# Kernel tuning notes

Measured on AMD Instinct MI355X. Metric: run time of the kernel, lower is better.

Reference implementation:

```python
import jax, jax.numpy as jnp
import numpy as np

PAD_TOKEN_ID = 0
EPS = 1e-12  # torch F.normalize eps

B_Q, L_Q = 64, 32
B_D, L_D = 512, 256
HID, OUT = 768, 128
VOCAB = 30522


def setup_inputs() -> dict:
    key = jax.random.key(0)
    k1, k2, k3, k4, k5 = jax.random.split(key, 5)
    return {
        "q_hidden": jax.random.normal(k1, (B_Q, L_Q, HID), dtype=jnp.float32),
        "d_hidden": jax.random.normal(k2, (B_D, L_D, HID), dtype=jnp.float32),
        "d_input_ids": jax.random.randint(k3, (B_D, L_D), 0, VOCAB, dtype=jnp.int32),
        "skiplist": jax.random.randint(k4, (64,), 0, VOCAB, dtype=jnp.int32),
        "W": jax.random.normal(k5, (OUT, HID), dtype=jnp.float32) * (HID ** -0.5),
    }


def _l2norm(x):
    n = jnp.sqrt(jnp.sum(x * x, axis=-1, keepdims=True))
    return x / jnp.maximum(n, EPS)


def reference(q_hidden, d_hidden, d_input_ids, skiplist, W):
    # query(): linear proj + L2 normalize      (B_q, L_q, F)
    Q = _l2norm(jnp.einsum("blh,fh->blf", q_hidden, W))
    # doc(): linear proj + L2 normalize + mask (B_d, L_d, F)
    D = _l2norm(jnp.einsum("blh,fh->blf", d_hidden, W))
    is_pad = d_input_ids == PAD_TOKEN_ID
    is_punct = jnp.any(d_input_ids[..., None] == skiplist, axis=-1)
    d_mask = (~is_pad) & (~is_punct)                     # (B_d, L_d)
    D = D * d_mask[..., None].astype(D.dtype)
    # forward(): reshape to (B, N, L, F) with B = min(B_q, B_d)
    B = min(q_hidden.shape[0], d_hidden.shape[0])
    Qr = Q.reshape(B, -1, L_Q, OUT)                      # (B, 1, L_q, F)
    Dr = D.reshape(B, -1, L_D, OUT)                      # (B, N_p, L_d, F)
    Mr = d_mask.reshape(B, -1, L_D)                      # (B, N_p, L_d)
    # similarity(): cosine MaxSim, Q @ D^T with broadcast over N_p
    sim = jnp.einsum("bqf,bndf->bnqd", Qr[:, 0], Dr)     # (B, N_p, L_q, L_d)
    sim = jnp.where(Mr[:, :, None, :], sim, -jnp.inf)
    sms = jnp.max(sim, axis=-1).mean(axis=-1)            # (B, N_p)
    return sms
```

## Files before the change

### kernel.cpp

```cpp
#include <hip/hip_runtime.h>
#include <stdint.h>

typedef float  f32x4 __attribute__((ext_vector_type(4)));
typedef short  s16x8 __attribute__((ext_vector_type(8)));
typedef unsigned int u32;
typedef unsigned short u16;
typedef unsigned int u32x4 __attribute__((ext_vector_type(4)));

#define HID 768
#define OUTF 128
#define LQ 32
#define LD 256

__device__ __forceinline__ u32 pk_rna(float lo, float hi) {
    u32 a = __builtin_bit_cast(u32, lo) + 0x8000u;
    u32 b = __builtin_bit_cast(u32, hi) + 0x8000u;
    return __builtin_amdgcn_perm(b, a, 0x07060302u);
}
__device__ __forceinline__ u16 f2bf(float x) {
    return (u16)((__builtin_bit_cast(u32, x) + 0x8000u) >> 16);
}
__device__ __forceinline__ s16x8 cvt8(f32x4 lo, f32x4 hi) {
    union { u32 u[4]; s16x8 v; } ua;
    ua.u[0] = pk_rna(lo[0], lo[1]);
    ua.u[1] = pk_rna(lo[2], lo[3]);
    ua.u[2] = pk_rna(hi[0], hi[1]);
    ua.u[3] = pk_rna(hi[2], hi[3]);
    return ua.v;
}

__global__ __launch_bounds__(256) void wconv(const float* __restrict__ W,
                                             u32* __restrict__ Wb3d) {
    int t = blockIdx.x * 256 + threadIdx.x;
    int j2   = t & 3;
    int lane = (t >> 2) & 63;
    int cf   = (t >> 8) & 7;
    int kk   = t >> 11;
    int l15 = lane & 15, g4 = lane >> 4;
    int f = cf * 16 + l15;
    int k = kk * 32 + g4 * 8 + j2 * 2;
    const float* src = W + (size_t)f * HID + k;
    Wb3d[t] = pk_rna(src[0], src[1]);
}

__global__ __launch_bounds__(256) void qproj(const float* __restrict__ qh,
                                             const u16* __restrict__ Wb3,
                                             u16* __restrict__ Qb) {
    const int b = blockIdx.x;
    const int tid = threadIdx.x;
    const int w = tid >> 6, lane = tid & 63, g = lane >> 4, l15 = lane & 15;

    f32x4 acc[2][2] = {};
    const float* A0 = qh + ((size_t)b * LQ + l15) * HID + g * 8;
    const float* A1 = A0 + 16 * HID;
    const u16* Bp = Wb3 + w * 1024 + lane * 8;

    for (int kk = 0; kk < 24; ++kk) {
        f32x4 x0 = *(const f32x4*)A0;
        f32x4 x1 = *(const f32x4*)(A0 + 4);
        f32x4 y0 = *(const f32x4*)A1;
        f32x4 y1 = *(const f32x4*)(A1 + 4);
        s16x8 b0 = *(const s16x8*)(Bp);
        s16x8 b1 = *(const s16x8*)(Bp + 512);
        s16x8 a0 = cvt8(x0, x1);
        s16x8 a1 = cvt8(y0, y1);
        acc[0][0] = __builtin_amdgcn_mfma_f32_16x16x32_bf16(a0, b0, acc[0][0], 0, 0, 0);
        acc[0][1] = __builtin_amdgcn_mfma_f32_16x16x32_bf16(a0, b1, acc[0][1], 0, 0, 0);
        acc[1][0] = __builtin_amdgcn_mfma_f32_16x16x32_bf16(a1, b0, acc[1][0], 0, 0, 0);
        acc[1][1] = __builtin_amdgcn_mfma_f32_16x16x32_bf16(a1, b1, acc[1][1], 0, 0, 0);
        A0 += 32; A1 += 32; Bp += 4096;
    }

    __shared__ float part[4][32];
    __shared__ float invl[32];
#pragma unroll
    for (int rf = 0; rf < 2; ++rf)
#pragma unroll
        for (int reg = 0; reg < 4; ++reg) {
            float ss = acc[rf][0][reg] * acc[rf][0][reg] + acc[rf][1][reg] * acc[rf][1][reg];
            ss += __shfl_xor(ss, 1); ss += __shfl_xor(ss, 2);
            ss += __shfl_xor(ss, 4); ss += __shfl_xor(ss, 8);
            if (l15 == 0) part[w][rf * 16 + g * 4 + reg] = ss;
        }
    __syncthreads();
    if (tid < 32) {
        float ss = part[0][tid] + part[1][tid] + part[2][tid] + part[3][tid];
        invl[tid] = 1.f / fmaxf(sqrtf(ss), 1e-12f);
    }
    __syncthreads();
#pragma unroll
    for (int rf = 0; rf < 2; ++rf)
#pragma unroll
        for (int cf = 0; cf < 2; ++cf)
#pragma unroll
            for (int reg = 0; reg < 4; ++reg) {
                int q = rf * 16 + g * 4 + reg;
                int f = w * 32 + cf * 16 + l15;
                Qb[(size_t)b * LQ * OUTF + q * OUTF + f] = f2bf(acc[rf][cf][reg] * invl[q]);
            }
}

__global__ __launch_bounds__(512, 2) void dmax(const float* __restrict__ dh,
                                               const int* __restrict__ ids,
                                               const int* __restrict__ skiplist,
                                               const u16* __restrict__ Wb3,
                                               const u16* __restrict__ Qb,
                                               float* __restrict__ out) {
    const int bid = blockIdx.x;
    const int tid = threadIdx.x;
    const int w = tid >> 6, lane = tid & 63, g4 = lane >> 4, l15 = lane & 15;
    const int qh_ = w >> 2;

    __shared__ __align__(16) u16 stg[3][12288];
    __shared__ __align__(16) u16 outb[2][2048];
    __shared__ __align__(16) float nrm[2][16][8];
    __shared__ float red[8][16];
    __shared__ int ms[512];
    __shared__ int sk[64];

#define PADOF(v) (((v) / 192) * 1536 + (((((v) % 192)) * 8) ^ ((((v) / 192) & 7) << 4)))
    const int pad0 = PADOF(2 * tid), pad1 = PADOF(2 * tid + 1024), pad2 = PADOF(2 * tid + 2048);

    const int swz = (l15 & 7) << 4, sw45 = swz & 48, sw6 = swz & 64;
    const int aoffE = l15 * 1536 + ((g4 * 16) ^ sw45) + sw6;
    const int aoffO = l15 * 1536 + ((g4 * 16) ^ sw45) + 64 - sw6;
    const int doffE = l15 * 256 + ((g4 * 16) ^ sw45) + sw6;
    const int doffO = l15 * 256 + ((g4 * 16) ^ sw45) + 64 - sw6;

    f32x4 LA0, LA1, LA2, LA3, LA4, LA5, LB0, LB1, LB2, LB3, LB4, LB5,
          LC0, LC1, LC2, LC3, LC4, LC5;
    s16x8 Qr0, Qr1, Qr2, Qr3;
    float rmaxH[4] = {-INFINITY, -INFINITY, -INFINITY, -INFINITY};

#define SLABBASE(sab) ((const char*)dh + (size_t)(bid + (((sab) >> 4) << 8)) * 786432 \
                       + (size_t)((sab) & 15) * 49152)

#define LISSUE(sab, S) { const char* gb_ = SLABBASE(sab) + 32 * tid; \
    S##0 = *(const f32x4*)(gb_);          S##1 = *(const f32x4*)(gb_ + 16); \
    S##2 = *(const f32x4*)(gb_ + 16384);  S##3 = *(const f32x4*)(gb_ + 16400); \
    S##4 = *(const f32x4*)(gb_ + 32768);  S##5 = *(const f32x4*)(gb_ + 32784); }

#define WSTORE(P, S) { char* sb_ = (char*)&stg[P][0]; u32x4 q_; \
    q_[0] = pk_rna(S##0[0], S##0[1]); q_[1] = pk_rna(S##0[2], S##0[3]); \
    q_[2] = pk_rna(S##1[0], S##1[1]); q_[3] = pk_rna(S##1[2], S##1[3]); \
    *(u32x4*)(sb_ + pad0) = q_; \
    q_[0] = pk_rna(S##2[0], S##2[1]); q_[1] = pk_rna(S##2[2], S##2[3]); \
    q_[2] = pk_rna(S##3[0], S##3[1]); q_[3] = pk_rna(S##3[2], S##3[3]); \
    *(u32x4*)(sb_ + pad1) = q_; \
    q_[0] = pk_rna(S##4[0], S##4[1]); q_[1] = pk_rna(S##4[2], S##4[3]); \
    q_[2] = pk_rna(S##5[0], S##5[1]); q_[3] = pk_rna(S##5[2], S##5[3]); \
    *(u32x4*)(sb_ + pad2) = q_; }

#define QLOAD(doc_) { const u16* qp_ = Qb + (size_t)((bid + (doc_) * 256) >> 3) * 4096 \
                      + (qh_ * 16 + l15) * 128 + g4 * 8; \
    Qr0 = *(const s16x8*)(qp_);      Qr1 = *(const s16x8*)(qp_ + 32); \
    Qr2 = *(const s16x8*)(qp_ + 64); Qr3 = *(const s16x8*)(qp_ + 96); }

#define GEMMN(P, s_) { \
    const char* Ab_ = (const char*)&stg[P][0]; \
    u16* ob_ = &outb[(s_) & 1][0]; \
    f32x4 ac0_ = {}, ac1_ = {}; \
    _Pragma("unroll") for (int kkp = 0; kkp < 12; ++kkp) { \
        s16x8 ae_ = *(const s16x8*)(Ab_ + aoffE + kkp * 128); \
        s16x8 ao_ = *(const s16x8*)(Ab_ + aoffO + kkp * 128); \
        ac0_ = __builtin_amdgcn_mfma_f32_16x16x32_bf16(ae_, Bf[2 * kkp],     ac0_, 0, 0, 0); \
        ac1_ = __builtin_amdgcn_mfma_f32_16x16x32_bf16(ao_, Bf[2 * kkp + 1], ac1_, 0, 0, 0); \
    } \
    f32x4 aG_ = ac0_ + ac1_; \
    _Pragma("unroll") for (int rg = 0; rg < 4; ++rg) { \
        float ss_ = aG_[rg] * aG_[rg]; \
        ss_ += __shfl_xor(ss_, 1); ss_ += __shfl_xor(ss_, 2); \
        ss_ += __shfl_xor(ss_, 4); ss_ += __shfl_xor(ss_, 8); \
        if (l15 == 0) nrm[(s_) & 1][g4 * 4 + rg][w] = ss_; \
        int dr_ = g4 * 4 + rg; \
        int of_ = (dr_ * 256 + (w * 16 + l15) * 2) ^ ((dr_ & 7) << 4); \
        *(u16*)((char*)ob_ + of_) = f2bf(aG_[rg]); \
    } }

#define TAIL(sb) { \
    if ((w & 3) == ((sb) & 3)) { \
        const char* Db_ = (const char*)&outb[(sb) & 1][0]; \
        s16x8 d0_ = *(const s16x8*)(Db_ + doffE); \
        s16x8 d1_ = *(const s16x8*)(Db_ + doffO); \
        s16x8 d2_ = *(const s16x8*)(Db_ + doffE + 128); \
        s16x8 d3_ = *(const s16x8*)(Db_ + doffO + 128); \
        f32x4 s2_ = {}; \
        s2_ = __builtin_amdgcn_mfma_f32_16x16x32_bf16(Qr0, d0_, s2_, 0, 0, 0); \
        s2_ = __builtin_amdgcn_mfma_f32_16x16x32_bf16(Qr1, d1_, s2_, 0, 0, 0); \
        s2_ = __builtin_amdgcn_mfma_f32_16x16x32_bf16(Qr2, d2_, s2_, 0, 0, 0); \
        s2_ = __builtin_amdgcn_mfma_f32_16x16x32_bf16(Qr3, d3_, s2_, 0, 0, 0); \
        f32x4 n0_ = *(const f32x4*)&nrm[(sb) & 1][l15][0]; \
        f32x4 n1_ = *(const f32x4*)&nrm[(sb) & 1][l15][4]; \
        float ssv_ = (n0_[0] + n0_[1] + n0_[2] + n0_[3]) \
                   + (n1_[0] + n1_[1] + n1_[2] + n1_[3]); \
        float inv_ = 1.f / fmaxf(sqrtf(ssv_), 1e-12f); \
        int keep_ = ms[(((sb) >> 4) << 8) + (((sb) & 15) << 4) + l15]; \
        _Pragma("unroll") for (int rg = 0; rg < 4; ++rg) { \
            float v_ = keep_ ? s2_[rg] * inv_ : -INFINITY; \
            rmaxH[rg] = fmaxf(rmaxH[rg], v_); } \
    } \
    if (((sb) & 15) == 15) { \
        _Pragma("unroll") for (int rg = 0; rg < 4; ++rg) { \
            float v_ = rmaxH[rg]; \
            v_ = fmaxf(v_, __shfl_xor(v_, 1)); v_ = fmaxf(v_, __shfl_xor(v_, 2)); \
            v_ = fmaxf(v_, __shfl_xor(v_, 4)); v_ = fmaxf(v_, __shfl_xor(v_, 8)); \
            if (l15 == 0) red[w][g4 * 4 + rg] = v_; \
            rmaxH[rg] = -INFINITY; } \
        asm volatile("s_waitcnt lgkmcnt(0)" ::: "memory"); \
        __builtin_amdgcn_s_barrier(); \
        if (tid < 32) { \
            int qi_ = tid & 15; \
            int base_ = (tid < 16) ? 0 : 4; \
            float m_ = fmaxf(fmaxf(red[base_][qi_], red[base_ + 1][qi_]), \
                             fmaxf(red[base_ + 2][qi_], red[base_ + 3][qi_])); \
            m_ += __shfl_xor(m_, 1); m_ += __shfl_xor(m_, 2); \
            m_ += __shfl_xor(m_, 4); m_ += __shfl_xor(m_, 8); \
            m_ += __shfl_xor(m_, 16); \
            if (tid == 0) out[bid + (((sb) >> 4) << 8)] = m_ * (1.f / 32.f); } \
        if ((sb) == 15) { QLOAD(1); } \
    } }

#define SLABSTEP(s_, PG_, PW_, RN_, RW_, doIssue_, doWr_) { \
    if (doIssue_) LISSUE((s_) + 3, RN_); \
    GEMMN(PG_, s_); \
    if (doWr_) WSTORE(PW_, RW_); \
    asm volatile("s_waitcnt lgkmcnt(0)" ::: "memory"); \
    __builtin_amdgcn_s_barrier(); \
    TAIL(s_); }

    LISSUE(0, LA);
    LISSUE(1, LB);
    LISSUE(2, LC);

    s16x8 Bf[24];
#pragma unroll
    for (int kk = 0; kk < 24; ++kk)
        Bf[kk] = *(const s16x8*)(Wb3 + (size_t)(kk * 8 + w) * 512 + lane * 8);

    if (tid < 64) sk[tid] = skiplist[tid];
    asm volatile("s_waitcnt lgkmcnt(0)" ::: "memory");
    __builtin_amdgcn_s_barrier();
    {
        int d_ = tid >> 8, r_ = tid & 255;
        int id_ = ids[(size_t)(bid + d_ * 256) * 256 + r_];
        int keep_ = (id_ != 0);
#pragma unroll
        for (int j = 0; j < 64; ++j) keep_ &= (id_ != sk[j]);
        ms[tid] = keep_;
    }
    WSTORE(0, LA);
    QLOAD(0);
    asm volatile("s_waitcnt lgkmcnt(0)" ::: "memory");
    __builtin_amdgcn_s_barrier();

    for (int j = 0; j < 10; ++j) {
        const int s0 = 3 * j;
        SLABSTEP(s0,     0, 1, LA, LB, true,        true);
        SLABSTEP(s0 + 1, 1, 2, LB, LC, true,        true);
        SLABSTEP(s0 + 2, 2, 0, LC, LA, s0 + 5 < 32, true);
    }
    SLABSTEP(30, 0, 1, LA, LB, false, true);
    SLABSTEP(31, 1, 2, LB, LC, false, false);
}

extern "C" void kernel_launch(void* const* d_in, const int* in_sizes, int n_in,
                              void* d_out, int out_size, void* d_ws, size_t ws_size,
                              hipStream_t stream) {
    const float* q_hidden = (const float*)d_in[0];
    const float* d_hidden = (const float*)d_in[1];
    const int*   d_ids    = (const int*)d_in[2];
    const int*   skiplist = (const int*)d_in[3];
    const float* W        = (const float*)d_in[4];
    float* out = (float*)d_out;

    u16* Wb3 = (u16*)d_ws;
    u16* Qb  = (u16*)((char*)d_ws + 256 * 1024);

    wconv<<<192, 256, 0, stream>>>(W, (u32*)Wb3);
    qproj<<<64, 256, 0, stream>>>(q_hidden, Wb3, Qb);
    dmax<<<256, 512, 0, stream>>>(d_hidden, d_ids, skiplist, Wb3, Qb, out);
}
```

Measured before the change: 102.9 us.

## Process slabs in pairs with four LDS stages to halve barriers

Restructures the dmax main loop from a three-stage one-slab-per-barrier pipeline to a four-buffer scheme that stages, projects and scores two slabs per barrier interval. Global loads for the next pair are issued while the current pair is projected, and the per-document max reduction moves out into a separate FLUSH step. This aims to cut the number of workgroup barriers per slab and give more independent MFMA work between syncs. In exchange it uses more LDS (four staging buffers), which may limit occupancy at two blocks per CU, and it keeps fewer register-held prefetches in flight.

```diff
diff --git a/kernel.cpp b/kernel.cpp
--- a/kernel.cpp
+++ b/kernel.cpp
@@ -111,9 +111,9 @@
     const int w = tid >> 6, lane = tid & 63, g4 = lane >> 4, l15 = lane & 15;
     const int qh_ = w >> 2;
 
-    __shared__ __align__(16) u16 stg[3][12288];
-    __shared__ __align__(16) u16 outb[2][2048];
-    __shared__ __align__(16) float nrm[2][16][8];
+    __shared__ __align__(16) u16 stg[4][12288];
+    __shared__ __align__(16) u16 outb[4][2048];
+    __shared__ __align__(16) float nrm[4][16][8];
     __shared__ float red[8][16];
     __shared__ int ms[512];
     __shared__ int sk[64];
@@ -127,8 +127,7 @@
     const int doffE = l15 * 256 + ((g4 * 16) ^ sw45) + sw6;
     const int doffO = l15 * 256 + ((g4 * 16) ^ sw45) + 64 - sw6;
 
-    f32x4 LA0, LA1, LA2, LA3, LA4, LA5, LB0, LB1, LB2, LB3, LB4, LB5,
-          LC0, LC1, LC2, LC3, LC4, LC5;
+    f32x4 LA0, LA1, LA2, LA3, LA4, LA5, LB0, LB1, LB2, LB3, LB4, LB5;
     s16x8 Qr0, Qr1, Qr2, Qr3;
     float rmaxH[4] = {-INFINITY, -INFINITY, -INFINITY, -INFINITY};
 
@@ -156,9 +155,9 @@
     Qr0 = *(const s16x8*)(qp_);      Qr1 = *(const s16x8*)(qp_ + 32); \
     Qr2 = *(const s16x8*)(qp_ + 64); Qr3 = *(const s16x8*)(qp_ + 96); }
 
-#define GEMMN(P, s_) { \
+#define GEMMN(P, OB) { \
     const char* Ab_ = (const char*)&stg[P][0]; \
-    u16* ob_ = &outb[(s_) & 1][0]; \
+    u16* ob_ = &outb[OB][0]; \
     f32x4 ac0_ = {}, ac1_ = {}; \
     _Pragma("unroll") for (int kkp = 0; kkp < 12; ++kkp) { \
         s16x8 ae_ = *(const s16x8*)(Ab_ + aoffE + kkp * 128); \
@@ -171,15 +170,15 @@
         float ss_ = aG_[rg] * aG_[rg]; \
         ss_ += __shfl_xor(ss_, 1); ss_ += __shfl_xor(ss_, 2); \
         ss_ += __shfl_xor(ss_, 4); ss_ += __shfl_xor(ss_, 8); \
-        if (l15 == 0) nrm[(s_) & 1][g4 * 4 + rg][w] = ss_; \
+        if (l15 == 0) nrm[OB][g4 * 4 + rg][w] = ss_; \
         int dr_ = g4 * 4 + rg; \
         int of_ = (dr_ * 256 + (w * 16 + l15) * 2) ^ ((dr_ & 7) << 4); \
         *(u16*)((char*)ob_ + of_) = f2bf(aG_[rg]); \
     } }
 
-#define TAIL(sb) { \
-    if ((w & 3) == ((sb) & 3)) { \
-        const char* Db_ = (const char*)&outb[(sb) & 1][0]; \
+#define TAILP(sb, OB, PR) { \
+    if ((w & 3) == (PR)) { \
+        const char* Db_ = (const char*)&outb[OB][0]; \
         s16x8 d0_ = *(const s16x8*)(Db_ + doffE); \
         s16x8 d1_ = *(const s16x8*)(Db_ + doffO); \
         s16x8 d2_ = *(const s16x8*)(Db_ + doffE + 128); \
@@ -189,8 +188,8 @@
         s2_ = __builtin_amdgcn_mfma_f32_16x16x32_bf16(Qr1, d1_, s2_, 0, 0, 0); \
         s2_ = __builtin_amdgcn_mfma_f32_16x16x32_bf16(Qr2, d2_, s2_, 0, 0, 0); \
         s2_ = __builtin_amdgcn_mfma_f32_16x16x32_bf16(Qr3, d3_, s2_, 0, 0, 0); \
-        f32x4 n0_ = *(const f32x4*)&nrm[(sb) & 1][l15][0]; \
-        f32x4 n1_ = *(const f32x4*)&nrm[(sb) & 1][l15][4]; \
+        f32x4 n0_ = *(const f32x4*)&nrm[OB][l15][0]; \
+        f32x4 n1_ = *(const f32x4*)&nrm[OB][l15][4]; \
         float ssv_ = (n0_[0] + n0_[1] + n0_[2] + n0_[3]) \
                    + (n1_[0] + n1_[1] + n1_[2] + n1_[3]); \
         float inv_ = 1.f / fmaxf(sqrtf(ssv_), 1e-12f); \
@@ -198,39 +197,29 @@
         _Pragma("unroll") for (int rg = 0; rg < 4; ++rg) { \
             float v_ = keep_ ? s2_[rg] * inv_ : -INFINITY; \
             rmaxH[rg] = fmaxf(rmaxH[rg], v_); } \
-    } \
-    if (((sb) & 15) == 15) { \
-        _Pragma("unroll") for (int rg = 0; rg < 4; ++rg) { \
-            float v_ = rmaxH[rg]; \
-            v_ = fmaxf(v_, __shfl_xor(v_, 1)); v_ = fmaxf(v_, __shfl_xor(v_, 2)); \
-            v_ = fmaxf(v_, __shfl_xor(v_, 4)); v_ = fmaxf(v_, __shfl_xor(v_, 8)); \
-            if (l15 == 0) red[w][g4 * 4 + rg] = v_; \
-            rmaxH[rg] = -INFINITY; } \
-        asm volatile("s_waitcnt lgkmcnt(0)" ::: "memory"); \
-        __builtin_amdgcn_s_barrier(); \
-        if (tid < 32) { \
-            int qi_ = tid & 15; \
-            int base_ = (tid < 16) ? 0 : 4; \
-            float m_ = fmaxf(fmaxf(red[base_][qi_], red[base_ + 1][qi_]), \
-                             fmaxf(red[base_ + 2][qi_], red[base_ + 3][qi_])); \
-            m_ += __shfl_xor(m_, 1); m_ += __shfl_xor(m_, 2); \
-            m_ += __shfl_xor(m_, 4); m_ += __shfl_xor(m_, 8); \
-            m_ += __shfl_xor(m_, 16); \
-            if (tid == 0) out[bid + (((sb) >> 4) << 8)] = m_ * (1.f / 32.f); } \
-        if ((sb) == 15) { QLOAD(1); } \
     } }
 
-#define SLABSTEP(s_, PG_, PW_, RN_, RW_, doIssue_, doWr_) { \
-    if (doIssue_) LISSUE((s_) + 3, RN_); \
-    GEMMN(PG_, s_); \
-    if (doWr_) WSTORE(PW_, RW_); \
+#define FLUSH(doc_) { \
+    _Pragma("unroll") for (int rg = 0; rg < 4; ++rg) { \
+        float v_ = rmaxH[rg]; \
+        v_ = fmaxf(v_, __shfl_xor(v_, 1)); v_ = fmaxf(v_, __shfl_xor(v_, 2)); \
+        v_ = fmaxf(v_, __shfl_xor(v_, 4)); v_ = fmaxf(v_, __shfl_xor(v_, 8)); \
+        if (l15 == 0) red[w][g4 * 4 + rg] = v_; \
+        rmaxH[rg] = -INFINITY; } \
     asm volatile("s_waitcnt lgkmcnt(0)" ::: "memory"); \
     __builtin_amdgcn_s_barrier(); \
-    TAIL(s_); }
+    if (tid < 32) { \
+        int qi_ = tid & 15; \
+        int base_ = (tid < 16) ? 0 : 4; \
+        float m_ = fmaxf(fmaxf(red[base_][qi_], red[base_ + 1][qi_]), \
+                         fmaxf(red[base_ + 2][qi_], red[base_ + 3][qi_])); \
+        m_ += __shfl_xor(m_, 1); m_ += __shfl_xor(m_, 2); \
+        m_ += __shfl_xor(m_, 4); m_ += __shfl_xor(m_, 8); \
+        m_ += __shfl_xor(m_, 16); \
+        if (tid == 0) out[bid + (doc_) * 256] = m_ * (1.f / 32.f); } }
 
     LISSUE(0, LA);
     LISSUE(1, LB);
-    LISSUE(2, LC);
 
     s16x8 Bf[24];
 #pragma unroll
@@ -249,18 +238,44 @@
         ms[tid] = keep_;
     }
     WSTORE(0, LA);
+    WSTORE(1, LB);
+    LISSUE(2, LA);
+    LISSUE(3, LB);
     QLOAD(0);
     asm volatile("s_waitcnt lgkmcnt(0)" ::: "memory");
     __builtin_amdgcn_s_barrier();
 
-    for (int j = 0; j < 10; ++j) {
-        const int s0 = 3 * j;
-        SLABSTEP(s0,     0, 1, LA, LB, true,        true);
-        SLABSTEP(s0 + 1, 1, 2, LB, LC, true,        true);
-        SLABSTEP(s0 + 2, 2, 0, LC, LA, s0 + 5 < 32, true);
-    }
-    SLABSTEP(30, 0, 1, LA, LB, false, true);
-    SLABSTEP(31, 1, 2, LB, LC, false, false);
+    for (int j = 0; j < 8; ++j) {
+        if (j > 0) {
+            TAILP(4 * j - 2, 2, 2);
+            TAILP(4 * j - 1, 3, 3);
+        }
+        WSTORE(2, LA);
+        WSTORE(3, LB);
+        if (j < 7) { LISSUE(4 * j + 4, LA); LISSUE(4 * j + 5, LB); }
+        GEMMN(0, 0);
+        GEMMN(1, 1);
+        asm volatile("s_waitcnt lgkmcnt(0)" ::: "memory");
+        __builtin_amdgcn_s_barrier();
+
+        if (j == 4) { FLUSH(0); QLOAD(1); }
+        TAILP(4 * j, 0, 0);
+        TAILP(4 * j + 1, 1, 1);
+        if (j < 7) {
+            WSTORE(0, LA);
+            WSTORE(1, LB);
+            LISSUE(4 * j + 6, LA);
+            LISSUE(4 * j + 7, LB);
+        }
+        GEMMN(2, 2);
+        GEMMN(3, 3);
+        asm volatile("s_waitcnt lgkmcnt(0)" ::: "memory");
+        __builtin_amdgcn_s_barrier();
+    }
+
+    TAILP(30, 2, 2);
+    TAILP(31, 3, 3);
+    FLUSH(1);
 }
 
 extern "C" void kernel_launch(void* const* d_in, const int* in_sizes, int n_in,
```

After: 107.1 us. +4.1%, slower.

## Shrink doc-slab pipeline from triple to double buffering in dmax

Applied to the files above, without the earlier changes.

Replaces the three register sets and three LDS staging buffers for the d_hidden slab pipeline with one register set and two LDS buffers. Each step now runs the GEMM on the current buffer, converts and stores the next slab into the other buffer, then issues the global load for the slab two ahead, with sched_barriers fixing the order. This saves 36 VGPRs and 24 KB of LDS, which may ease register pressure or allow more residency. The cost is a shorter prefetch distance, so global load latency is less well hidden.

```diff
diff --git a/kernel.cpp b/kernel.cpp
--- a/kernel.cpp
+++ b/kernel.cpp
@@ -111,7 +111,7 @@
     const int w = tid >> 6, lane = tid & 63, g4 = lane >> 4, l15 = lane & 15;
     const int qh_ = w >> 2;
 
-    __shared__ __align__(16) u16 stg[3][12288];
+    __shared__ __align__(16) u16 stg[2][12288];
     __shared__ __align__(16) u16 outb[2][2048];
     __shared__ __align__(16) float nrm[2][16][8];
     __shared__ float red[8][16];
@@ -127,28 +127,27 @@
     const int doffE = l15 * 256 + ((g4 * 16) ^ sw45) + sw6;
     const int doffO = l15 * 256 + ((g4 * 16) ^ sw45) + 64 - sw6;
 
-    f32x4 LA0, LA1, LA2, LA3, LA4, LA5, LB0, LB1, LB2, LB3, LB4, LB5,
-          LC0, LC1, LC2, LC3, LC4, LC5;
+    f32x4 LA0, LA1, LA2, LA3, LA4, LA5;
     s16x8 Qr0, Qr1, Qr2, Qr3;
     float rmaxH[4] = {-INFINITY, -INFINITY, -INFINITY, -INFINITY};
 
 #define SLABBASE(sab) ((const char*)dh + (size_t)(bid + (((sab) >> 4) << 8)) * 786432 \
                        + (size_t)((sab) & 15) * 49152)
 
-#define LISSUE(sab, S) { const char* gb_ = SLABBASE(sab) + 32 * tid; \
-    S##0 = *(const f32x4*)(gb_);          S##1 = *(const f32x4*)(gb_ + 16); \
-    S##2 = *(const f32x4*)(gb_ + 16384);  S##3 = *(const f32x4*)(gb_ + 16400); \
-    S##4 = *(const f32x4*)(gb_ + 32768);  S##5 = *(const f32x4*)(gb_ + 32784); }
-
-#define WSTORE(P, S) { char* sb_ = (char*)&stg[P][0]; u32x4 q_; \
-    q_[0] = pk_rna(S##0[0], S##0[1]); q_[1] = pk_rna(S##0[2], S##0[3]); \
-    q_[2] = pk_rna(S##1[0], S##1[1]); q_[3] = pk_rna(S##1[2], S##1[3]); \
+#define LISSUE(sab) { const char* gb_ = SLABBASE(sab) + 32 * tid; \
+    LA0 = *(const f32x4*)(gb_);          LA1 = *(const f32x4*)(gb_ + 16); \
+    LA2 = *(const f32x4*)(gb_ + 16384);  LA3 = *(const f32x4*)(gb_ + 16400); \
+    LA4 = *(const f32x4*)(gb_ + 32768);  LA5 = *(const f32x4*)(gb_ + 32784); }
+
+#define WSTORE(P) { char* sb_ = (char*)&stg[P][0]; u32x4 q_; \
+    q_[0] = pk_rna(LA0[0], LA0[1]); q_[1] = pk_rna(LA0[2], LA0[3]); \
+    q_[2] = pk_rna(LA1[0], LA1[1]); q_[3] = pk_rna(LA1[2], LA1[3]); \
     *(u32x4*)(sb_ + pad0) = q_; \
-    q_[0] = pk_rna(S##2[0], S##2[1]); q_[1] = pk_rna(S##2[2], S##2[3]); \
-    q_[2] = pk_rna(S##3[0], S##3[1]); q_[3] = pk_rna(S##3[2], S##3[3]); \
+    q_[0] = pk_rna(LA2[0], LA2[1]); q_[1] = pk_rna(LA2[2], LA2[3]); \
+    q_[2] = pk_rna(LA3[0], LA3[1]); q_[3] = pk_rna(LA3[2], LA3[3]); \
     *(u32x4*)(sb_ + pad1) = q_; \
-    q_[0] = pk_rna(S##4[0], S##4[1]); q_[1] = pk_rna(S##4[2], S##4[3]); \
-    q_[2] = pk_rna(S##5[0], S##5[1]); q_[3] = pk_rna(S##5[2], S##5[3]); \
+    q_[0] = pk_rna(LA4[0], LA4[1]); q_[1] = pk_rna(LA4[2], LA4[3]); \
+    q_[2] = pk_rna(LA5[0], LA5[1]); q_[3] = pk_rna(LA5[2], LA5[3]); \
     *(u32x4*)(sb_ + pad2) = q_; }
 
 #define QLOAD(doc_) { const u16* qp_ = Qb + (size_t)((bid + (doc_) * 256) >> 3) * 4096 \
@@ -220,17 +219,17 @@
         if ((sb) == 15) { QLOAD(1); } \
     } }
 
-#define SLABSTEP(s_, PG_, PW_, RN_, RW_, doIssue_, doWr_) { \
-    if (doIssue_) LISSUE((s_) + 3, RN_); \
+#define SLABSTEP(s_, PG_) { \
     GEMMN(PG_, s_); \
-    if (doWr_) WSTORE(PW_, RW_); \
+    __builtin_amdgcn_sched_barrier(0); \
+    if ((s_) + 1 < 32) WSTORE(((s_) + 1) & 1); \
+    __builtin_amdgcn_sched_barrier(0); \
+    if ((s_) + 2 < 32) LISSUE((s_) + 2); \
     asm volatile("s_waitcnt lgkmcnt(0)" ::: "memory"); \
     __builtin_amdgcn_s_barrier(); \
     TAIL(s_); }
 
-    LISSUE(0, LA);
-    LISSUE(1, LB);
-    LISSUE(2, LC);
+    LISSUE(0);
 
     s16x8 Bf[24];
 #pragma unroll
@@ -248,19 +247,16 @@
         for (int j = 0; j < 64; ++j) keep_ &= (id_ != sk[j]);
         ms[tid] = keep_;
     }
-    WSTORE(0, LA);
+    WSTORE(0);
+    LISSUE(1);
     QLOAD(0);
     asm volatile("s_waitcnt lgkmcnt(0)" ::: "memory");
     __builtin_amdgcn_s_barrier();
 
-    for (int j = 0; j < 10; ++j) {
-        const int s0 = 3 * j;
-        SLABSTEP(s0,     0, 1, LA, LB, true,        true);
-        SLABSTEP(s0 + 1, 1, 2, LB, LC, true,        true);
-        SLABSTEP(s0 + 2, 2, 0, LC, LA, s0 + 5 < 32, true);
-    }
-    SLABSTEP(30, 0, 1, LA, LB, false, true);
-    SLABSTEP(31, 1, 2, LB, LC, false, false);
+    for (int j = 0; j < 16; ++j) {
+        SLABSTEP(2 * j, 0);
+        SLABSTEP(2 * j + 1, 1);
+    }
 }
 
 extern "C" void kernel_launch(void* const* d_in, const int* in_sizes, int n_in,
```

New measurement: 100.4 us, median of 2. 1.02x faster.
